# Kernel tuning notes

Measured on AMD Instinct MI355X. Metric: run time of the kernel, lower is better.

The kernel has to match this reference:

```python
import jax, jax.numpy as jnp
import numpy as np

N = 50000      # nodes
E = 800000     # edges (avg degree 16)
IN = 128       # in_dim == hidden_dim*num_heads so residuals fire
D = 32         # hidden_dim (per-head)
H = 4          # num_heads
OUT = 64       # out_dim (final layer has 1 head)
NEG_SLOPE = 0.2
LN_EPS = 1e-5


def setup_inputs() -> dict:
    key = jax.random.key(0)
    ks = jax.random.split(key, 16)
    rn = lambda k, s: jax.random.normal(k, s, jnp.float32) * 0.05
    return {
        "features": jax.random.normal(ks[0], (N, IN), jnp.float32),
        "edge_weight": jax.random.uniform(ks[1], (E,), jnp.float32),
        "src": jax.random.randint(ks[2], (E,), 0, N),
        "dst": jax.random.randint(ks[3], (E,), 0, N),
        "W0": rn(ks[4], (IN, H * D)), "al0": rn(ks[5], (H, D)), "ar0": rn(ks[6], (H, D)), "lam0": jnp.float32(1.0),
        "W1": rn(ks[7], (H * D, H * D)), "al1": rn(ks[8], (H, D)), "ar1": rn(ks[9], (H, D)), "lam1": jnp.float32(1.0),
        "W2": rn(ks[10], (H * D, OUT)), "al2": rn(ks[11], (1, OUT)), "ar2": rn(ks[12], (1, OUT)), "lam2": jnp.float32(1.0),
        "g0": jnp.ones((H * D,), jnp.float32), "b0": jnp.zeros((H * D,), jnp.float32),
        "g1": jnp.ones((H * D,), jnp.float32), "b1": jnp.zeros((H * D,), jnp.float32),
    }


def _gat_layer(h, W, al, ar, lam, src, dst, ew):
    n = h.shape[0]
    heads, d = al.shape
    ft = (h @ W).reshape(n, heads, d)                      # [N,H,D]
    el = jnp.sum(ft * al[None], axis=-1)                   # [N,H]
    er = jnp.sum(ft * ar[None], axis=-1)                   # [N,H]
    e = el[src] + er[dst] + lam * ew[:, None]              # [E,H] u_add_v + weight bias
    e = jax.nn.leaky_relu(e, NEG_SLOPE)
    # edge softmax over incoming edges of each dst node
    m = jax.ops.segment_max(e, dst, num_segments=n)        # [N,H]
    ex = jnp.exp(e - m[dst])
    s = jax.ops.segment_sum(ex, dst, num_segments=n)       # [N,H]
    a = ex / s[dst]                                        # [E,H]
    # u_mul_e + sum aggregation
    msg = ft[src] * a[:, :, None]                          # [E,H,D]
    return jax.ops.segment_sum(msg, dst, num_segments=n)   # [N,H,D]


def _layer_norm(x, g, b):
    mu = jnp.mean(x, axis=-1, keepdims=True)
    var = jnp.mean((x - mu) ** 2, axis=-1, keepdims=True)
    return (x - mu) * jax.lax.rsqrt(var + LN_EPS) * g + b


def _forward(features, edge_weight, src, dst,
             W0, al0, ar0, lam0, W1, al1, ar1, lam1, W2, al2, ar2, lam2,
             g0, b0, g1, b1):
    n = features.shape[0]
    h = features
    # layer 0
    h1 = _gat_layer(h, W0, al0, ar0, lam0, src, dst, edge_weight)
    h1 = jax.nn.elu(h1).reshape(n, -1)
    h1 = _layer_norm(h1, g0, b0)
    if h1.shape == h.shape:
        h1 = h1 + h
    # layer 1
    h2 = _gat_layer(h1, W1, al1, ar1, lam1, src, dst, edge_weight)
    h2 = jax.nn.elu(h2).reshape(n, -1)
    h2 = _layer_norm(h2, g1, b1)
    h2 = h2 + h1
    # layer 2 (single head, no activation)
    out = _gat_layer(h2, W2, al2, ar2, lam2, src, dst, edge_weight).reshape(n, -1)
    return out


def reference(features, edge_weight, src, dst,
              W0, al0, ar0, lam0, W1, al1, ar1, lam1, W2, al2, ar2, lam2,
              g0, b0, g1, b1):
    # eval mode: dropout off and _add_noise is identity, so noisy == clean
    h_clean = _forward(features, edge_weight, src, dst,
                       W0, al0, ar0, lam0, W1, al1, ar1, lam1, W2, al2, ar2, lam2,
                       g0, b0, g1, b1)
    return (h_clean, h_clean)
```

## Files before the change

kernel.cpp:

```cpp
#include <hip/hip_runtime.h>

#define NEG_SLOPE 0.2f
#define LN_EPS 1e-5f

typedef __attribute__((ext_vector_type(8))) short bf16x8;
typedef __attribute__((ext_vector_type(4))) float f32x4;

__device__ inline unsigned short f2bf(float f) {
    unsigned u = __float_as_uint(f);
    unsigned r = u + 0x7FFFu + ((u >> 16) & 1u);
    return (unsigned short)(r >> 16);
}

__device__ inline void unpack8(uint4 u, float* f) {
    f[0] = __uint_as_float(u.x << 16);
    f[1] = __uint_as_float(u.x & 0xFFFF0000u);
    f[2] = __uint_as_float(u.y << 16);
    f[3] = __uint_as_float(u.y & 0xFFFF0000u);
    f[4] = __uint_as_float(u.z << 16);
    f[5] = __uint_as_float(u.z & 0xFFFF0000u);
    f[6] = __uint_as_float(u.w << 16);
    f[7] = __uint_as_float(u.w & 0xFFFF0000u);
}


__global__ __launch_bounds__(256) void zero_wt_kernel(
    uint4* __restrict__ z, int nz, int ZB,
    const float* __restrict__ W0, const float* __restrict__ W1,
    const float* __restrict__ W2, unsigned short* __restrict__ Wt0,
    unsigned short* __restrict__ Wt1, unsigned short* __restrict__ Wt2) {
    int bid = blockIdx.x;
    if (bid < ZB) {
        int base = bid * 1024 + threadIdx.x;
        #pragma unroll
        for (int j = 0; j < 4; ++j) {
            int idx = base + j * 256;
            if (idx < nz) z[idx] = make_uint4(0, 0, 0, 0);
        }
    } else {
        int row = (bid - ZB) * 2 + (threadIdx.x >> 7);
        int k = threadIdx.x & 127;
        if (row < 128) {
            Wt0[row * 128 + k] = f2bf(W0[k * 128 + row]);
        } else if (row < 256) {
            int c = row - 128;
            Wt1[c * 128 + k] = f2bf(W1[k * 128 + c]);
        } else {
            int c = row - 256;
            Wt2[c * 128 + k] = f2bf(W2[k * 64 + c]);
        }
    }
}


__global__ __launch_bounds__(256) void hist_gemm0(
    const int* __restrict__ dst, int* __restrict__ counts, int* __restrict__ rank,
    int E, int RB, const float* __restrict__ Ap, const unsigned short* __restrict__ Wt,
    const float* __restrict__ al, const float* __restrict__ ar,
    unsigned short* __restrict__ ftb, float* __restrict__ el,
    float* __restrict__ er, int n) {
    constexpr int LDA = 136;
    constexpr int NT = 8, H = 4, D = 32;
    __shared__ unsigned short As[64 * LDA];
    __shared__ unsigned short Ws[NT * 16 * LDA];
    int t = threadIdx.x;
    if (blockIdx.x < RB) {
        int i = blockIdx.x * 256 + t;
        if (i < E) rank[i] = atomicAdd(&counts[dst[i] * 16], 1);
        return;
    }
    int row0 = (blockIdx.x - RB) * 64;

    const float4* A4 = (const float4*)Ap;
    #pragma unroll
    for (int j = 0; j < 8; ++j) {
        int idx = t + j * 256;
        int r = idx >> 5;
        int c4 = idx & 31;
        int row = row0 + r;
        float4 v = (row < n) ? A4[(size_t)row * 32 + c4] : make_float4(0.f, 0.f, 0.f, 0.f);
        unsigned p0 = (unsigned)f2bf(v.x) | ((unsigned)f2bf(v.y) << 16);
        unsigned p1 = (unsigned)f2bf(v.z) | ((unsigned)f2bf(v.w) << 16);
        *(uint2*)&As[r * LDA + c4 * 4] = make_uint2(p0, p1);
    }
    const uint4* Wg = (const uint4*)Wt;
    #pragma unroll
    for (int j = 0; j < NT; ++j) {
        int idx = t + j * 256;
        int r = idx >> 4;
        int c8 = idx & 15;
        *(uint4*)&Ws[r * LDA + c8 * 8] = Wg[idx];
    }
    __syncthreads();

    int w = t >> 6, lane = t & 63;
    int m = lane & 15, q = lane >> 4;
    f32x4 acc[NT] = {};
    const unsigned short* ap = &As[(w * 16 + m) * LDA + q * 8];
    #pragma unroll
    for (int kk = 0; kk < 4; ++kk) {
        bf16x8 a = *(const bf16x8*)(ap + kk * 32);
        #pragma unroll
        for (int nt = 0; nt < NT; ++nt) {
            bf16x8 b = *(const bf16x8*)&Ws[(nt * 16 + m) * LDA + kk * 32 + q * 8];
            acc[nt] = __builtin_amdgcn_mfma_f32_16x16x32_bf16(a, b, acc[nt], 0, 0, 0);
        }
    }

    float alv[NT], arv[NT];
    #pragma unroll
    for (int nt = 0; nt < NT; ++nt) {
        alv[nt] = al[nt * 16 + m];
        arv[nt] = ar[nt * 16 + m];
    }

    int orow = row0 + w * 16 + q * 4;
    #pragma unroll
    for (int r = 0; r < 4; ++r) {
        int row = orow + r;
        float pl[H] = {}, pr[H] = {};
        #pragma unroll
        for (int nt = 0; nt < NT; ++nt) {
            int h = (nt * 16) / D;
            pl[h] = fmaf(acc[nt][r], alv[nt], pl[h]);
            pr[h] = fmaf(acc[nt][r], arv[nt], pr[h]);
        }
        #pragma unroll
        for (int off = 1; off < 16; off <<= 1) {
            #pragma unroll
            for (int h = 0; h < H; ++h) {
                pl[h] += __shfl_xor(pl[h], off, 64);
                pr[h] += __shfl_xor(pr[h], off, 64);
            }
        }
        if (row < n) {
            #pragma unroll
            for (int nt = 0; nt < NT; ++nt)
                ftb[(size_t)row * 128 + nt * 16 + m] = f2bf(acc[nt][r]);
            if (m < H) {
                float vl = pl[0], vr = pr[0];
                #pragma unroll
                for (int h = 1; h < H; ++h)
                    if (m == h) { vl = pl[h]; vr = pr[h]; }
                el[row * H + m] = vl;
                er[row * H + m] = vr;
            }
        }
    }
}


__global__ __launch_bounds__(256) void scan1_kernel(const int* __restrict__ counts,
                                                    int* __restrict__ bsum, int n) {
    __shared__ int lds[256];
    int t = threadIdx.x;
    int i = blockIdx.x * 256 + t;
    lds[t] = (i < n) ? counts[i * 16] : 0;
    __syncthreads();
    for (int off = 128; off > 0; off >>= 1) {
        int v = (t < off) ? lds[t + off] : 0;
        __syncthreads();
        if (t < off) lds[t] += v;
        __syncthreads();
    }
    if (t == 0) bsum[blockIdx.x] = lds[0];
}


__global__ __launch_bounds__(256) void scan3_kernel(const int* __restrict__ counts,
                                                    const int* __restrict__ bsum,
                                                    int* __restrict__ rowptr, int n,
                                                    int E, int nscan) {
    __shared__ int lds[256];
    int t = threadIdx.x;
    lds[t] = (t < nscan) ? bsum[t] : 0;
    __syncthreads();
    for (int off = 1; off < 256; off <<= 1) {
        int v = (t >= off) ? lds[t - off] : 0;
        __syncthreads();
        lds[t] += v;
        __syncthreads();
    }
    int boff = (blockIdx.x > 0) ? lds[blockIdx.x - 1] : 0;
    __syncthreads();
    int i = blockIdx.x * 256 + t;
    int c = (i < n) ? counts[i * 16] : 0;
    lds[t] = c;
    __syncthreads();
    for (int off = 1; off < 256; off <<= 1) {
        int v = (t >= off) ? lds[t - off] : 0;
        __syncthreads();
        lds[t] += v;
        __syncthreads();
    }
    if (i < n) rowptr[i] = boff + lds[t] - c;
    if (i == n) rowptr[n] = E;
}


__global__ __launch_bounds__(256) void place_kernel(
    const int* __restrict__ src, const int* __restrict__ dst,
    const float* __restrict__ ew, const int* __restrict__ rowptr,
    const int* __restrict__ rank, unsigned* __restrict__ edge_p, int E) {
    int i = blockIdx.x * 256 + threadIdx.x;
    if (i < E) {
        int p = rowptr[dst[i]] + rank[i];
        edge_p[p] = ((unsigned)f2bf(ew[i]) << 16) | (unsigned)src[i];
    }
}


__device__ inline void accum8(float* ax, uint4 u, float p) {
    ax[0] = fmaf(p, __uint_as_float(u.x << 16), ax[0]);
    ax[1] = fmaf(p, __uint_as_float(u.x & 0xFFFF0000u), ax[1]);
    ax[2] = fmaf(p, __uint_as_float(u.y << 16), ax[2]);
    ax[3] = fmaf(p, __uint_as_float(u.y & 0xFFFF0000u), ax[3]);
    ax[4] = fmaf(p, __uint_as_float(u.z << 16), ax[4]);
    ax[5] = fmaf(p, __uint_as_float(u.z & 0xFFFF0000u), ax[5]);
    ax[6] = fmaf(p, __uint_as_float(u.w << 16), ax[6]);
    ax[7] = fmaf(p, __uint_as_float(u.w & 0xFFFF0000u), ax[7]);
}

__device__ inline void accum4(float* ax, uint2 u, float p) {
    ax[0] = fmaf(p, __uint_as_float(u.x << 16), ax[0]);
    ax[1] = fmaf(p, __uint_as_float(u.x & 0xFFFF0000u), ax[1]);
    ax[2] = fmaf(p, __uint_as_float(u.y << 16), ax[2]);
    ax[3] = fmaf(p, __uint_as_float(u.y & 0xFFFF0000u), ax[3]);
}

template <int K>
__device__ inline void agg_batch(const uint4* __restrict__ ftb4,
                                 const float* __restrict__ el, unsigned ev, int j,
                                 int li, int head, float erv, float lam, float* ax,
                                 float& s) {
    unsigned ee[K];
    uint4 uu[K];
    float ll[K];
    #pragma unroll
    for (int k = 0; k < K; ++k) ee[k] = __shfl(ev, j + k, 16);
    #pragma unroll
    for (int k = 0; k < K; ++k) {
        unsigned sn = ee[k] & 0xFFFFu;
        uu[k] = ftb4[(size_t)sn * 16 + li];
        ll[k] = el[sn * 4 + head];
    }
    #pragma unroll
    for (int k = 0; k < K; ++k) {
        float v = ll[k] + erv + lam * __uint_as_float(ee[k] & 0xFFFF0000u);
        v = fmaxf(v, NEG_SLOPE * v);
        float p = __expf(v);
        accum8(ax, uu[k], p);
        s += p;
    }
}

template <int K>
__device__ inline void agg_batch_out(const uint2* __restrict__ ftb2,
                                     const float* __restrict__ el, unsigned ev,
                                     int j, int li, float erv, float lam, float* ax,
                                     float& s) {
    unsigned ee[K];
    uint2 uu[K];
    float ll[K];
    #pragma unroll
    for (int k = 0; k < K; ++k) ee[k] = __shfl(ev, j + k, 16);
    #pragma unroll
    for (int k = 0; k < K; ++k) {
        unsigned sn = ee[k] & 0xFFFFu;
        uu[k] = ftb2[(size_t)sn * 16 + li];
        ll[k] = el[sn];
    }
    #pragma unroll
    for (int k = 0; k < K; ++k) {
        float v = ll[k] + erv + lam * __uint_as_float(ee[k] & 0xFFFF0000u);
        v = fmaxf(v, NEG_SLOPE * v);
        float p = __expf(v);
        accum4(ax, uu[k], p);
        s += p;
    }
}


template <bool PREV32, int VER>
__global__ __launch_bounds__(256) void fused_agg_gemm(
    const int* __restrict__ rowptr, const unsigned* __restrict__ edge_p,
    const uint4* __restrict__ ftb4, const float* __restrict__ el_in,
    const float* __restrict__ er_in, const float* __restrict__ lam_p,
    const float* __restrict__ g, const float* __restrict__ b,
    const void* __restrict__ prevp, uint4* __restrict__ houtb,
    const unsigned short* __restrict__ Wt, const float* __restrict__ al,
    const float* __restrict__ ar, unsigned short* __restrict__ ftb_out,
    float* __restrict__ el_out, float* __restrict__ er_out, int n) {
    constexpr int LDA = 136;
    __shared__ unsigned short As[16 * LDA];
    __shared__ float red[2][4][16];
    int t = threadIdx.x;
    int node0 = blockIdx.x * 16;
    int nl = t >> 4;
    int node = node0 + nl;
    int li = t & 15;

    if (node < n) {
        int head = li >> 2;
        float lam = lam_p[0];
        float erv = er_in[node * 4 + head];
        int s0 = rowptr[node], s1 = rowptr[node + 1];
        float ax[8] = {};
        float s = 0.f;

        for (int base = s0; base < s1; base += 16) {
            int m = s1 - base;
            if (m > 16) m = 16;
            unsigned ev = (li < m) ? edge_p[base + li] : 0u;
            int j = 0;
            for (; j + 8 <= m; j += 8)
                agg_batch<8>(ftb4, el_in, ev, j, li, head, erv, lam, ax, s);
            if (j + 4 <= m) {
                agg_batch<4>(ftb4, el_in, ev, j, li, head, erv, lam, ax, s);
                j += 4;
            }
            for (; j < m; ++j)
                agg_batch<1>(ftb4, el_in, ev, j, li, head, erv, lam, ax, s);
        }

        float inv = (s > 0.f) ? 1.f / s : 0.f;
        float x[8];
        float sum = 0.f, sq = 0.f;
        #pragma unroll
        for (int d = 0; d < 8; ++d) {
            float v = ax[d] * inv;
            v = (v > 0.f) ? v : expm1f(v);
            x[d] = v;
            sum += v;
            sq += v * v;
        }
        #pragma unroll
        for (int off = 1; off < 16; off <<= 1) {
            sum += __shfl_xor(sum, off, 16);
            sq += __shfl_xor(sq, off, 16);
        }
        float mu = sum * (1.f / 128.f);
        float var = sq * (1.f / 128.f) - mu * mu;
        float rs = rsqrtf(var + LN_EPS);

        const float4* g4 = (const float4*)g;
        const float4* b4 = (const float4*)b;
        float pv[8];
        if constexpr (PREV32) {
            const float4* p4 = (const float4*)prevp;
            #pragma unroll
            for (int h = 0; h < 2; ++h) {
                float4 v = p4[(size_t)node * 32 + li * 2 + h];
                pv[h * 4 + 0] = v.x; pv[h * 4 + 1] = v.y;
                pv[h * 4 + 2] = v.z; pv[h * 4 + 3] = v.w;
            }
        } else {
            unpack8(((const uint4*)prevp)[(size_t)node * 16 + li], pv);
        }
        float y[8];
        #pragma unroll
        for (int h = 0; h < 2; ++h) {
            float4 gv = g4[li * 2 + h];
            float4 bv = b4[li * 2 + h];
            y[h * 4 + 0] = (x[h * 4 + 0] - mu) * rs * gv.x + bv.x + pv[h * 4 + 0];
            y[h * 4 + 1] = (x[h * 4 + 1] - mu) * rs * gv.y + bv.y + pv[h * 4 + 1];
            y[h * 4 + 2] = (x[h * 4 + 2] - mu) * rs * gv.z + bv.z + pv[h * 4 + 2];
            y[h * 4 + 3] = (x[h * 4 + 3] - mu) * rs * gv.w + bv.w + pv[h * 4 + 3];
        }
        uint4 o;
        o.x = (unsigned)f2bf(y[0]) | ((unsigned)f2bf(y[1]) << 16);
        o.y = (unsigned)f2bf(y[2]) | ((unsigned)f2bf(y[3]) << 16);
        o.z = (unsigned)f2bf(y[4]) | ((unsigned)f2bf(y[5]) << 16);
        o.w = (unsigned)f2bf(y[6]) | ((unsigned)f2bf(y[7]) << 16);
        if constexpr (VER == 1) houtb[(size_t)node * 16 + li] = o;
        *(uint4*)&As[nl * LDA + li * 8] = o;
    } else {
        *(uint4*)&As[nl * LDA + li * 8] = make_uint4(0, 0, 0, 0);
    }
    __syncthreads();

    int w = t >> 6, lane = t & 63;
    int m = lane & 15, q = lane >> 4;
    if constexpr (VER == 1) {
        f32x4 acc[2] = {};
        #pragma unroll
        for (int kk = 0; kk < 4; ++kk) {
            bf16x8 a = *(const bf16x8*)&As[m * LDA + kk * 32 + q * 8];
            #pragma unroll
            for (int nt = 0; nt < 2; ++nt) {
                int col = w * 32 + nt * 16 + m;
                bf16x8 bb = *(const bf16x8*)&Wt[(size_t)col * 128 + kk * 32 + q * 8];
                acc[nt] = __builtin_amdgcn_mfma_f32_16x16x32_bf16(a, bb, acc[nt], 0, 0, 0);
            }
        }
        float alv0 = al[w * 32 + m], alv1 = al[w * 32 + 16 + m];
        float arv0 = ar[w * 32 + m], arv1 = ar[w * 32 + 16 + m];
        #pragma unroll
        for (int r = 0; r < 4; ++r) {
            int row = node0 + q * 4 + r;
            float pl = acc[0][r] * alv0 + acc[1][r] * alv1;
            float pr = acc[0][r] * arv0 + acc[1][r] * arv1;
            #pragma unroll
            for (int off = 1; off < 16; off <<= 1) {
                pl += __shfl_xor(pl, off, 64);
                pr += __shfl_xor(pr, off, 64);
            }
            if (row < n) {
                ftb_out[(size_t)row * 128 + w * 32 + m] = f2bf(acc[0][r]);
                ftb_out[(size_t)row * 128 + w * 32 + 16 + m] = f2bf(acc[1][r]);
                if (m == 0) {
                    el_out[row * 4 + w] = pl;
                    er_out[row * 4 + w] = pr;
                }
            }
        }
    } else {
        f32x4 acc = {};
        #pragma unroll
        for (int kk = 0; kk < 4; ++kk) {
            bf16x8 a = *(const bf16x8*)&As[m * LDA + kk * 32 + q * 8];
            int col = w * 16 + m;
            bf16x8 bb = *(const bf16x8*)&Wt[(size_t)col * 128 + kk * 32 + q * 8];
            acc = __builtin_amdgcn_mfma_f32_16x16x32_bf16(a, bb, acc, 0, 0, 0);
        }
        float alv = al[w * 16 + m], arv = ar[w * 16 + m];
        #pragma unroll
        for (int r = 0; r < 4; ++r) {
            int row = node0 + q * 4 + r;
            float pl = acc[r] * alv;
            float pr = acc[r] * arv;
            #pragma unroll
            for (int off = 1; off < 16; off <<= 1) {
                pl += __shfl_xor(pl, off, 64);
                pr += __shfl_xor(pr, off, 64);
            }
            if (row < n) ftb_out[(size_t)row * 64 + w * 16 + m] = f2bf(acc[r]);
            if (m == 0) {
                red[0][w][q * 4 + r] = pl;
                red[1][w][q * 4 + r] = pr;
            }
        }
        __syncthreads();
        if (t < 16) {
            int row = node0 + t;
            if (row < n) {
                el_out[row] = red[0][0][t] + red[0][1][t] + red[0][2][t] + red[0][3][t];
                er_out[row] = red[1][0][t] + red[1][1][t] + red[1][2][t] + red[1][3][t];
            }
        }
    }
}


__global__ __launch_bounds__(256) void gat_agg_out(
    const int* __restrict__ rowptr, const unsigned* __restrict__ edge_p,
    const uint2* __restrict__ ftb2, const float* __restrict__ el,
    const float* __restrict__ er, const float* __restrict__ lam_p,
    float* __restrict__ out, int n) {
    int node = blockIdx.x * 16 + (threadIdx.x >> 4);
    if (node >= n) return;
    int li = threadIdx.x & 15;
    float lam = lam_p[0];
    float erv = er[node];
    int s0 = rowptr[node], s1 = rowptr[node + 1];
    float ax[4] = {};
    float s = 0.f;

    for (int base = s0; base < s1; base += 16) {
        int m = s1 - base;
        if (m > 16) m = 16;
        unsigned ev = (li < m) ? edge_p[base + li] : 0u;
        int j = 0;
        for (; j + 8 <= m; j += 8)
            agg_batch_out<8>(ftb2, el, ev, j, li, erv, lam, ax, s);
        if (j + 4 <= m) {
            agg_batch_out<4>(ftb2, el, ev, j, li, erv, lam, ax, s);
            j += 4;
        }
        for (; j < m; ++j)
            agg_batch_out<1>(ftb2, el, ev, j, li, erv, lam, ax, s);
    }

    float inv = (s > 0.f) ? 1.f / s : 0.f;
    float4 y;
    y.x = ax[0] * inv;
    y.y = ax[1] * inv;
    y.z = ax[2] * inv;
    y.w = ax[3] * inv;
    ((float4*)out)[(size_t)node * 16 + li] = y;
    ((float4*)out)[(size_t)(n + node) * 16 + li] = y;
}


extern "C" void kernel_launch(void* const* d_in, const int* in_sizes, int n_in,
                              void* d_out, int out_size, void* d_ws, size_t ws_size,
                              hipStream_t stream) {
    const float* features = (const float*)d_in[0];
    const float* edge_weight = (const float*)d_in[1];
    const int* src = (const int*)d_in[2];
    const int* dst = (const int*)d_in[3];
    const float* W0 = (const float*)d_in[4];
    const float* al0 = (const float*)d_in[5];
    const float* ar0 = (const float*)d_in[6];
    const float* lam0 = (const float*)d_in[7];
    const float* W1 = (const float*)d_in[8];
    const float* al1 = (const float*)d_in[9];
    const float* ar1 = (const float*)d_in[10];
    const float* lam1 = (const float*)d_in[11];
    const float* W2 = (const float*)d_in[12];
    const float* al2 = (const float*)d_in[13];
    const float* ar2 = (const float*)d_in[14];
    const float* lam2 = (const float*)d_in[15];
    const float* g0 = (const float*)d_in[16];
    const float* b0 = (const float*)d_in[17];
    const float* g1 = (const float*)d_in[18];
    const float* b1 = (const float*)d_in[19];

    const int N = in_sizes[0] / 128;
    const int E = in_sizes[1];

    char* w = (char*)d_ws;
    size_t o = 0;
    auto carve = [&](size_t bytes) {
        char* p = w + o;
        o += (bytes + 255) & ~(size_t)255;
        return p;
    };
    int* counts = (int*)carve((size_t)N * 64);
    int* rowptr = (int*)carve((size_t)(N + 1) * 4);
    int* bsum = (int*)carve(256 * 4);
    int* rank = (int*)carve((size_t)E * 4);
    unsigned* edge_p = (unsigned*)carve((size_t)E * 4);
    unsigned short* ftbA = (unsigned short*)carve((size_t)N * 128 * 2);
    unsigned short* ftbB = (unsigned short*)carve((size_t)N * 128 * 2);
    unsigned short* ftbC = (unsigned short*)carve((size_t)N * 64 * 2);
    unsigned short* h1 = (unsigned short*)carve((size_t)N * 128 * 2);
    float* elA = (float*)carve((size_t)N * 4 * 4);
    float* erA = (float*)carve((size_t)N * 4 * 4);
    float* elB = (float*)carve((size_t)N * 4 * 4);
    float* erB = (float*)carve((size_t)N * 4 * 4);
    float* elC = (float*)carve((size_t)N * 4);
    float* erC = (float*)carve((size_t)N * 4);
    unsigned short* Wt0 = (unsigned short*)carve(128 * 128 * 2);
    unsigned short* Wt1 = (unsigned short*)carve(128 * 128 * 2);
    unsigned short* Wt2 = (unsigned short*)carve(64 * 128 * 2);

    const int nscan = (N + 255) / 256;
    const int ngemm = (N + 63) / 64;
    const int nagg = (N + 15) / 16;
    const int RB = (E + 255) / 256;
    const int nz = N * 4;
    const int ZB = (nz + 1023) / 1024;

    zero_wt_kernel<<<ZB + 160, 256, 0, stream>>>((uint4*)counts, nz, ZB,
                                                 W0, W1, W2, Wt0, Wt1, Wt2);
    hist_gemm0<<<RB + ngemm, 256, 0, stream>>>(dst, counts, rank, E, RB,
                                               features, Wt0, al0, ar0,
                                               ftbA, elA, erA, N);
    scan1_kernel<<<nscan, 256, 0, stream>>>(counts, bsum, N);
    scan3_kernel<<<(N + 1 + 255) / 256, 256, 0, stream>>>(counts, bsum, rowptr, N, E,
                                                          nscan);
    place_kernel<<<RB, 256, 0, stream>>>(src, dst, edge_weight, rowptr, rank,
                                         edge_p, E);
    fused_agg_gemm<true, 1><<<nagg, 256, 0, stream>>>(
        rowptr, edge_p, (const uint4*)ftbA, elA, erA, lam0, g0, b0, features,
        (uint4*)h1, Wt1, al1, ar1, ftbB, elB, erB, N);
    fused_agg_gemm<false, 2><<<nagg, 256, 0, stream>>>(
        rowptr, edge_p, (const uint4*)ftbB, elB, erB, lam1, g1, b1, h1,
        nullptr, Wt2, al2, ar2, ftbC, elC, erC, N);
    gat_agg_out<<<nagg, 256, 0, stream>>>(rowptr, edge_p, (const uint2*)ftbC,
                                          elC, erC, lam2, (float*)d_out, N);
}
```

Baseline: 295.8 us.

## Sort nodes by in-degree into a permutation to balance aggregation blocks

Builds a degree histogram during the scan and a prefix over degree bins, then places node ids into a perm array ordered by descending in-degree (capped at 63). The aggregation and fused GEMM kernels process nodes in perm order, so the 16 nodes sharing a block have similar edge counts and the divergence and tail imbalance from mixed degrees shrinks. The cost is an extra indirection on every node index, scattered writes of ftb, el, er and the output rows, and a few more atomics in the preprocessing kernels. The 16-row tiles fed to the GEMM also hold non-contiguous nodes.

```diff
diff --git a/kernel.cpp b/kernel.cpp
--- a/kernel.cpp
+++ b/kernel.cpp
@@ -151,12 +151,17 @@
 
 
 __global__ __launch_bounds__(256) void scan1_kernel(const int* __restrict__ counts,
-                                                    int* __restrict__ bsum, int n) {
+                                                    int* __restrict__ bsum,
+                                                    int* __restrict__ dhist, int n) {
     __shared__ int lds[256];
+    __shared__ int hbin[64];
     int t = threadIdx.x;
+    if (t < 64) hbin[t] = 0;
     int i = blockIdx.x * 256 + t;
-    lds[t] = (i < n) ? counts[i * 16] : 0;
+    int c = (i < n) ? counts[i * 16] : 0;
+    lds[t] = c;
     __syncthreads();
+    if (i < n) atomicAdd(&hbin[63 - (c < 63 ? c : 63)], 1);
     for (int off = 128; off > 0; off >>= 1) {
         int v = (t < off) ? lds[t + off] : 0;
         __syncthreads();
@@ -164,13 +169,19 @@
         __syncthreads();
     }
     if (t == 0) bsum[blockIdx.x] = lds[0];
+    if (t < 64) {
+        int h = hbin[t];
+        if (h) atomicAdd(&dhist[t], h);
+    }
 }
 
 
 __global__ __launch_bounds__(256) void scan3_kernel(const int* __restrict__ counts,
                                                     const int* __restrict__ bsum,
-                                                    int* __restrict__ rowptr, int n,
-                                                    int E, int nscan) {
+                                                    int* __restrict__ rowptr,
+                                                    const int* __restrict__ dhist,
+                                                    int* __restrict__ dbase,
+                                                    int n, int E, int nscan) {
     __shared__ int lds[256];
     int t = threadIdx.x;
     lds[t] = (t < nscan) ? bsum[t] : 0;
@@ -195,17 +206,50 @@
     }
     if (i < n) rowptr[i] = boff + lds[t] - c;
     if (i == n) rowptr[n] = E;
+    if (blockIdx.x == 0 && t < 64) {
+        int v = dhist[t];
+        int x = v;
+        #pragma unroll
+        for (int off = 1; off < 64; off <<= 1) {
+            int u = __shfl_up(x, off, 64);
+            if (t >= off) x += u;
+        }
+        dbase[t] = x - v;
+    }
 }
 
 
 __global__ __launch_bounds__(256) void place_kernel(
     const int* __restrict__ src, const int* __restrict__ dst,
     const float* __restrict__ ew, const int* __restrict__ rowptr,
-    const int* __restrict__ rank, unsigned* __restrict__ edge_p, int E) {
-    int i = blockIdx.x * 256 + threadIdx.x;
-    if (i < E) {
-        int p = rowptr[dst[i]] + rank[i];
-        edge_p[p] = ((unsigned)f2bf(ew[i]) << 16) | (unsigned)src[i];
+    const int* __restrict__ rank, unsigned* __restrict__ edge_p,
+    const int* __restrict__ dbase, int* __restrict__ dcount,
+    int* __restrict__ perm, int E, int EB, int N) {
+    __shared__ int lbin[64];
+    __shared__ int lbase[64];
+    int bid = blockIdx.x;
+    int t = threadIdx.x;
+    if (bid < EB) {
+        int i = bid * 256 + t;
+        if (i < E) {
+            int p = rowptr[dst[i]] + rank[i];
+            edge_p[p] = ((unsigned)f2bf(ew[i]) << 16) | (unsigned)src[i];
+        }
+    } else {
+        if (t < 64) lbin[t] = 0;
+        __syncthreads();
+        int nidx = (bid - EB) * 256 + t;
+        bool valid = nidx < N;
+        int key = 0, myoff = 0;
+        if (valid) {
+            int deg = rowptr[nidx + 1] - rowptr[nidx];
+            key = 63 - (deg < 63 ? deg : 63);
+            myoff = atomicAdd(&lbin[key], 1);
+        }
+        __syncthreads();
+        if (t < 64) lbase[t] = lbin[t] ? atomicAdd(&dcount[t], lbin[t]) : 0;
+        __syncthreads();
+        if (valid) perm[dbase[key] + lbase[key] + myoff] = nidx;
     }
 }
 
@@ -284,23 +328,25 @@
 template <bool PREV32, int VER>
 __global__ __launch_bounds__(256) void fused_agg_gemm(
     const int* __restrict__ rowptr, const unsigned* __restrict__ edge_p,
-    const uint4* __restrict__ ftb4, const float* __restrict__ el_in,
-    const float* __restrict__ er_in, const float* __restrict__ lam_p,
-    const float* __restrict__ g, const float* __restrict__ b,
-    const void* __restrict__ prevp, uint4* __restrict__ houtb,
-    const unsigned short* __restrict__ Wt, const float* __restrict__ al,
-    const float* __restrict__ ar, unsigned short* __restrict__ ftb_out,
-    float* __restrict__ el_out, float* __restrict__ er_out, int n) {
+    const int* __restrict__ perm, const uint4* __restrict__ ftb4,
+    const float* __restrict__ el_in, const float* __restrict__ er_in,
+    const float* __restrict__ lam_p, const float* __restrict__ g,
+    const float* __restrict__ b, const void* __restrict__ prevp,
+    uint4* __restrict__ houtb, const unsigned short* __restrict__ Wt,
+    const float* __restrict__ al, const float* __restrict__ ar,
+    unsigned short* __restrict__ ftb_out, float* __restrict__ el_out,
+    float* __restrict__ er_out, int n) {
     constexpr int LDA = 136;
     __shared__ unsigned short As[16 * LDA];
     __shared__ float red[2][4][16];
     int t = threadIdx.x;
     int node0 = blockIdx.x * 16;
     int nl = t >> 4;
-    int node = node0 + nl;
+    int gid = node0 + nl;
     int li = t & 15;
 
-    if (node < n) {
+    if (gid < n) {
+        int node = perm[gid];
         int head = li >> 2;
         float lam = lam_p[0];
         float erv = er_in[node * 4 + head];
@@ -397,7 +443,7 @@
         float arv0 = ar[w * 32 + m], arv1 = ar[w * 32 + 16 + m];
         #pragma unroll
         for (int r = 0; r < 4; ++r) {
-            int row = node0 + q * 4 + r;
+            int gr = node0 + q * 4 + r;
             float pl = acc[0][r] * alv0 + acc[1][r] * alv1;
             float pr = acc[0][r] * arv0 + acc[1][r] * arv1;
             #pragma unroll
@@ -405,7 +451,8 @@
                 pl += __shfl_xor(pl, off, 64);
                 pr += __shfl_xor(pr, off, 64);
             }
-            if (row < n) {
+            if (gr < n) {
+                int row = perm[gr];
                 ftb_out[(size_t)row * 128 + w * 32 + m] = f2bf(acc[0][r]);
                 ftb_out[(size_t)row * 128 + w * 32 + 16 + m] = f2bf(acc[1][r]);
                 if (m == 0) {
@@ -426,7 +473,7 @@
         float alv = al[w * 16 + m], arv = ar[w * 16 + m];
         #pragma unroll
         for (int r = 0; r < 4; ++r) {
-            int row = node0 + q * 4 + r;
+            int gr = node0 + q * 4 + r;
             float pl = acc[r] * alv;
             float pr = acc[r] * arv;
             #pragma unroll
@@ -434,7 +481,7 @@
                 pl += __shfl_xor(pl, off, 64);
                 pr += __shfl_xor(pr, off, 64);
             }
-            if (row < n) ftb_out[(size_t)row * 64 + w * 16 + m] = f2bf(acc[r]);
+            if (gr < n) ftb_out[(size_t)perm[gr] * 64 + w * 16 + m] = f2bf(acc[r]);
             if (m == 0) {
                 red[0][w][q * 4 + r] = pl;
                 red[1][w][q * 4 + r] = pr;
@@ -442,8 +489,9 @@
         }
         __syncthreads();
         if (t < 16) {
-            int row = node0 + t;
-            if (row < n) {
+            int gr = node0 + t;
+            if (gr < n) {
+                int row = perm[gr];
                 el_out[row] = red[0][0][t] + red[0][1][t] + red[0][2][t] + red[0][3][t];
                 er_out[row] = red[1][0][t] + red[1][1][t] + red[1][2][t] + red[1][3][t];
             }
@@ -454,11 +502,12 @@
 
 __global__ __launch_bounds__(256) void gat_agg_out(
     const int* __restrict__ rowptr, const unsigned* __restrict__ edge_p,
-    const uint2* __restrict__ ftb2, const float* __restrict__ el,
-    const float* __restrict__ er, const float* __restrict__ lam_p,
-    float* __restrict__ out, int n) {
-    int node = blockIdx.x * 16 + (threadIdx.x >> 4);
-    if (node >= n) return;
+    const int* __restrict__ perm, const uint2* __restrict__ ftb2,
+    const float* __restrict__ el, const float* __restrict__ er,
+    const float* __restrict__ lam_p, float* __restrict__ out, int n) {
+    int gid = blockIdx.x * 16 + (threadIdx.x >> 4);
+    if (gid >= n) return;
+    int node = perm[gid];
     int li = threadIdx.x & 15;
     float lam = lam_p[0];
     float erv = er[node];
@@ -527,10 +576,14 @@
         return p;
     };
     int* counts = (int*)carve((size_t)N * 64);
+    int* dhist = (int*)carve(256);
+    int* dcount = (int*)carve(256);
     int* rowptr = (int*)carve((size_t)(N + 1) * 4);
     int* bsum = (int*)carve(256 * 4);
+    int* dbase = (int*)carve(256);
     int* rank = (int*)carve((size_t)E * 4);
     unsigned* edge_p = (unsigned*)carve((size_t)E * 4);
+    int* perm = (int*)carve((size_t)N * 4);
     unsigned short* ftbA = (unsigned short*)carve((size_t)N * 128 * 2);
     unsigned short* ftbB = (unsigned short*)carve((size_t)N * 128 * 2);
     unsigned short* ftbC = (unsigned short*)carve((size_t)N * 64 * 2);
@@ -549,7 +602,7 @@
     const int ngemm = (N + 63) / 64;
     const int nagg = (N + 15) / 16;
     const int RB = (E + 255) / 256;
-    const int nz = N * 4;
+    const int nz = N * 4 + 32;
     const int ZB = (nz + 1023) / 1024;
 
     zero_wt_kernel<<<ZB + 160, 256, 0, stream>>>((uint4*)counts, nz, ZB,
@@ -557,17 +610,17 @@
     hist_gemm0<<<RB + ngemm, 256, 0, stream>>>(dst, counts, rank, E, RB,
                                                features, Wt0, al0, ar0,
                                                ftbA, elA, erA, N);
-    scan1_kernel<<<nscan, 256, 0, stream>>>(counts, bsum, N);
-    scan3_kernel<<<(N + 1 + 255) / 256, 256, 0, stream>>>(counts, bsum, rowptr, N, E,
-                                                          nscan);
-    place_kernel<<<RB, 256, 0, stream>>>(src, dst, edge_weight, rowptr, rank,
-                                         edge_p, E);
+    scan1_kernel<<<nscan, 256, 0, stream>>>(counts, bsum, dhist, N);
+    scan3_kernel<<<(N + 1 + 255) / 256, 256, 0, stream>>>(counts, bsum, rowptr,
+                                                          dhist, dbase, N, E, nscan);
+    place_kernel<<<RB + nscan, 256, 0, stream>>>(src, dst, edge_weight, rowptr, rank,
+                                                 edge_p, dbase, dcount, perm, E, RB, N);
     fused_agg_gemm<true, 1><<<nagg, 256, 0, stream>>>(
-        rowptr, edge_p, (const uint4*)ftbA, elA, erA, lam0, g0, b0, features,
+        rowptr, edge_p, perm, (const uint4*)ftbA, elA, erA, lam0, g0, b0, features,
         (uint4*)h1, Wt1, al1, ar1, ftbB, elB, erB, N);
     fused_agg_gemm<false, 2><<<nagg, 256, 0, stream>>>(
-        rowptr, edge_p, (const uint4*)ftbB, elB, erB, lam1, g1, b1, h1,
+        rowptr, edge_p, perm, (const uint4*)ftbB, elB, erB, lam1, g1, b1, h1,
         nullptr, Wt2, al2, ar2, ftbC, elC, erC, N);
-    gat_agg_out<<<nagg, 256, 0, stream>>>(rowptr, edge_p, (const uint2*)ftbC,
+    gat_agg_out<<<nagg, 256, 0, stream>>>(rowptr, edge_p, perm, (const uint2*)ftbC,
                                           elC, erC, lam2, (float*)d_out, N);
 }
```

Result: no change. 290.1 us (-1.9%).
